# Performance work log

Measured on AMD Instinct MI355X. Metric: run time of the kernel, lower is better.

Reference implementation:

```python
import jax, jax.numpy as jnp
import numpy as np

B, S, H, F, E, TOP_K = 4, 2048, 768, 3072, 8, 2


def setup_inputs() -> dict:
    key = jax.random.key(0)
    ks = jax.random.split(key, 6)
    x = jax.random.normal(ks[0], (B, S, H), dtype=jnp.float32)
    Wr = jax.random.normal(ks[1], (E, H), dtype=jnp.float32) * 0.02
    Wi = jax.random.normal(ks[2], (E, F, H), dtype=jnp.float32) * 0.02
    bi = jnp.zeros((E, F), dtype=jnp.float32)
    Wo = jax.random.normal(ks[3], (E, H, F), dtype=jnp.float32) * 0.02
    bo = jnp.zeros((E, H), dtype=jnp.float32)
    return {"x": x, "Wr": Wr, "Wi": Wi, "bi": bi, "Wo": Wo, "bo": bo}


def reference(x, Wr, Wi, bi, Wo, bo):
    # x: [B, S, H] -> tokens [T, H]
    xf = x.reshape(-1, x.shape[-1])  # [T, H]

    # Router: linear (no bias), eval mode (no noise), temperature=1.0
    router_logits = jnp.einsum('th,eh->te', xf, Wr)  # [T, E]
    topk_vals, topk_idx = jax.lax.top_k(router_logits, TOP_K)  # [T, K]
    routing_weights = jax.nn.softmax(topk_vals, axis=-1)  # normalize over top-k

    # All experts on all tokens (forward_all_experts, parallel computation)
    h = jnp.einsum('th,efh->etf', xf, Wi) + bi[:, None, :]  # [E, T, F]
    h = jax.nn.gelu(h, approximate=False)  # BERT gelu (erf)
    expert_out = jnp.einsum('etf,ehf->eth', h, Wo) + bo[:, None, :]  # [E, T, H]
    expert_out = jnp.transpose(expert_out, (1, 0, 2))  # [T, E, H]

    # Gather top-k expert outputs per token and combine with routing weights
    gathered = jnp.take_along_axis(expert_out, topk_idx[:, :, None], axis=1)  # [T, K, H]
    out = jnp.einsum('tk,tkh->th', routing_weights, gathered)
    return out.reshape(x.shape)
```

## Files before the change

kernel.cpp:

```cpp
#include <hip/hip_runtime.h>
#include <hip/hip_bf16.h>
#include <cstdint>
#include <cstddef>

#define T_TOK 8192
#define HDIM  768
#define FDIM  3072
#define NEXP  8

typedef __attribute__((ext_vector_type(8))) __bf16 bf16x8;
typedef __attribute__((ext_vector_type(4))) float  f32x4;

static __device__ __forceinline__ f32x4 mfma16(bf16x8 a, bf16x8 b, f32x4 c) {
  return __builtin_amdgcn_mfma_f32_16x16x32_bf16(a, b, c, 0, 0, 0);
}

static __device__ __forceinline__ unsigned short f2b(float f) {
  return __builtin_bit_cast(unsigned short, (__bf16)f);
}

static __device__ __forceinline__ float gelu_f(float x) {
  float x2 = x * x;
  float y = x * (0.7978845608f + 0.0356774081f * x2);
  float ay = __builtin_fabsf(y);
  float z = __builtin_amdgcn_exp2f(ay * -2.885390082f);
  float t = (1.0f - z) * __builtin_amdgcn_rcpf(1.0f + z);
  t = __builtin_copysignf(t, y);
  return 0.5f * x * (1.0f + t);
}

static constexpr size_t OFF_XB   = 0;
static constexpr size_t OFF_WIB  = OFF_XB  + (size_t)T_TOK * HDIM * 2;
static constexpr size_t OFF_WOB  = OFF_WIB + (size_t)NEXP * FDIM * HDIM * 2;
static constexpr size_t OFF_HBUF = OFF_WOB + (size_t)NEXP * HDIM * FDIM * 2;
static constexpr size_t OFF_META = OFF_HBUF + (size_t)2 * T_TOK * FDIM * 2;
static constexpr size_t OFF_TOKE = OFF_META + 256;
static constexpr size_t OFF_TOKW = OFF_TOKE + 65536;
static constexpr size_t OFF_PTOK = OFF_TOKW + 65536;
static constexpr size_t OFF_PW   = OFF_PTOK + 65536;
static constexpr size_t OFF_TILE = OFF_PW + 65536;
static constexpr size_t OFF_STAGE = 0;

__global__ __launch_bounds__(256) void cvt_kernel(const float* __restrict__ s,
                                                  unsigned short* __restrict__ d, int n4) {
  int i = blockIdx.x * 256 + threadIdx.x;
  int stride = gridDim.x * 256;
  for (; i < n4; i += stride) {
    float4 v = ((const float4*)s)[i];
    ushort4 o;
    o.x = f2b(v.x); o.y = f2b(v.y); o.z = f2b(v.z); o.w = f2b(v.w);
    ((ushort4*)d)[i] = o;
  }
}

__global__ __launch_bounds__(256) void router_kernel(const float* __restrict__ x,
                                                     const float* __restrict__ Wr,
                                                     int* __restrict__ tok_e,
                                                     float* __restrict__ tok_w,
                                                     unsigned short* __restrict__ xb) {
  __shared__ float wr[NEXP * HDIM];
  int tid = threadIdx.x;
  for (int i = tid; i < NEXP * HDIM; i += 256) wr[i] = Wr[i];
  __syncthreads();
  int lane = tid & 63;
  int wv = tid >> 6;
  int t = blockIdx.x * 4 + wv;
  const float* xr = x + (size_t)t * HDIM;
  unsigned short* xbr = xb + (size_t)t * HDIM;
  float p[NEXP];
#pragma unroll
  for (int e = 0; e < NEXP; ++e) p[e] = 0.f;
  for (int j = 0; j < HDIM / 64; ++j) {
    float xv = xr[j * 64 + lane];
    xbr[j * 64 + lane] = f2b(xv);
#pragma unroll
    for (int e = 0; e < NEXP; ++e) p[e] += xv * wr[e * HDIM + j * 64 + lane];
  }
#pragma unroll
  for (int e = 0; e < NEXP; ++e) {
    float v = p[e];
    for (int off = 32; off; off >>= 1) v += __shfl_xor(v, off);
    p[e] = v;
  }
  if (lane == 0) {
    float v0 = -1e30f, v1 = -1e30f; int i0 = 0, i1 = 0;
#pragma unroll
    for (int e = 0; e < NEXP; ++e) {
      float v = p[e];
      if (v > v0) { v1 = v0; i1 = i0; v0 = v; i0 = e; }
      else if (v > v1) { v1 = v; i1 = e; }
    }
    float ew = expf(v1 - v0);
    float w0 = 1.0f / (1.0f + ew);
    float w1 = ew * w0;
    tok_e[t * 2 + 0] = i0; tok_w[t * 2 + 0] = w0;
    tok_e[t * 2 + 1] = i1; tok_w[t * 2 + 1] = w1;
  }
}

__global__ __launch_bounds__(256) void count_kernel(const int* __restrict__ tok_e,
                                                    int* __restrict__ counts) {
  __shared__ int h[NEXP];
  int tid = threadIdx.x;
  if (tid < NEXP) h[tid] = 0;
  __syncthreads();
  int i = blockIdx.x * 256 + tid;
  atomicAdd(&h[tok_e[i]], 1);
  __syncthreads();
  if (tid < NEXP && h[tid] > 0) atomicAdd(&counts[tid], h[tid]);
}

__global__ void scan_build_kernel(const int* __restrict__ counts, int* __restrict__ basep,
                                  int* __restrict__ tile_e, int* __restrict__ tile_mt,
                                  int* __restrict__ ntiles) {
  if (threadIdx.x != 0 || blockIdx.x != 0) return;
  int s = 0;
  for (int e = 0; e < NEXP; ++e) { basep[e] = s; s += counts[e]; }
  int n = 0;
  for (int e = 0; e < NEXP; ++e) {
    int nmt = (counts[e] + 255) >> 8;
    for (int m = 0; m < nmt; ++m) { tile_e[n] = e; tile_mt[n] = m; ++n; }
  }
  ntiles[0] = n;
}

__global__ __launch_bounds__(256) void scatter_kernel(const int* __restrict__ tok_e,
                                                      const float* __restrict__ tok_w,
                                                      const int* __restrict__ base,
                                                      int* __restrict__ cursor,
                                                      int* __restrict__ pair_tok,
                                                      float* __restrict__ pair_w) {
  __shared__ int h[NEXP], bstart[NEXP];
  int tid = threadIdx.x;
  if (tid < NEXP) h[tid] = 0;
  __syncthreads();
  int i = blockIdx.x * 256 + tid;
  int e = tok_e[i];
  int r = atomicAdd(&h[e], 1);
  __syncthreads();
  if (tid < NEXP) bstart[tid] = (h[tid] > 0) ? atomicAdd(&cursor[tid], h[tid]) : 0;
  __syncthreads();
  int pos = base[e] + bstart[e] + r;
  pair_tok[pos] = i;
  pair_w[pos] = tok_w[i];
}

template <int MODE>
__global__ __launch_bounds__(512, 2) void moe_gemm(
    const unsigned short* __restrict__ abase,
    const unsigned short* __restrict__ wbase,
    const float* __restrict__ bias,
    const int* __restrict__ counts, const int* __restrict__ base,
    const int* __restrict__ pair_tok, const float* __restrict__ pair_w,
    const int* __restrict__ tile_e, const int* __restrict__ tile_mt,
    const int* __restrict__ ntiles,
    unsigned short* __restrict__ hbuf, float* __restrict__ stage) {
  constexpr int K   = MODE ? FDIM : HDIM;
  constexpr int N   = MODE ? HDIM : FDIM;
  constexpr int NT  = K / 64;
  constexpr int NTC = N / 256;

  const int xcd = blockIdx.x & 7;
  const int slot = blockIdx.x >> 3;
  const int mtl = slot % 9;
  const int nt = slot / 9;
  const int ntl = ntiles[0];
  const int q = ntl >> 3, r = ntl & 7;
  const int cnt = q + (xcd < r ? 1 : 0);
  if (mtl >= cnt) return;
  const int gt = xcd * q + (xcd < r ? xcd : r) + mtl;
  const int e = tile_e[gt];
  const int mt = tile_mt[gt];
  const int ne = counts[e];
  const int pb = base[e];

  extern __shared__ char smem[];

  const int tid = threadIdx.x;
  const int lane = tid & 63;
  const int wv = tid >> 6;
  const int wm = wv >> 2;
  const int wn = wv & 3;
  const int l15 = lane & 15;
  const int lkb = (lane >> 4) * 16;

  const int crow = tid >> 3;
  const int ck = tid & 7;
  const int swz = (ck ^ (crow & 7)) * 16;
  const char* aS[4]; const char* bS[4];
#pragma unroll
  for (int i = 0; i < 4; ++i) {
    int gr = mt * 256 + i * 64 + crow; if (gr > ne - 1) gr = ne - 1;
    if constexpr (MODE == 0) {
      int tok = pair_tok[pb + gr] >> 1;
      aS[i] = (const char*)abase + (size_t)tok * (HDIM * 2) + swz;
    } else {
      aS[i] = (const char*)abase + (size_t)(pb + gr) * (FDIM * 2) + swz;
    }
    int br = nt * 256 + i * 64 + crow;
    bS[i] = (const char*)wbase + ((size_t)e * N * K + (size_t)br * K) * 2 + swz;
  }

  auto STAGE = [&](int c, int t) {
    if (t < NT) {
      const char* src = (c < 4 ? aS[c] : bS[c - 4]) + t * 128;
      char* dst = smem + (size_t)((t & 1) * 65536 + c * 8192 + tid * 16);
      __builtin_amdgcn_global_load_lds(
          (const __attribute__((address_space(1))) void*)src,
          (__attribute__((address_space(3))) void*)dst, 16, 0, 0);
    }
  };

  bf16x8 aR[8], bR0[4], bR1[4];
  f32x4 acc[8][4];
#pragma unroll
  for (int mi = 0; mi < 8; ++mi)
#pragma unroll
    for (int ni = 0; ni < 4; ++ni) acc[mi][ni] = (f32x4){0.f, 0.f, 0.f, 0.f};

  auto READA = [&](int cb, int h) {
#pragma unroll
    for (int m2 = 0; m2 < 4; ++m2)
#pragma unroll
      for (int k2 = 0; k2 < 2; ++k2) {
        int lr = wm * 128 + (h * 4 + m2) * 16 + l15;
        int cbyte = k2 * 64 + lkb;
        aR[m2 * 2 + k2] =
            *(const bf16x8*)(smem + cb + lr * 128 + (cbyte ^ ((lr & 7) << 4)));
      }
  };
  auto READB = [&](int cb, int h, bf16x8* bR) {
#pragma unroll
    for (int n2 = 0; n2 < 2; ++n2)
#pragma unroll
      for (int k2 = 0; k2 < 2; ++k2) {
        int lr = wn * 64 + (h * 2 + n2) * 16 + l15;
        int cbyte = k2 * 64 + lkb;
        bR[n2 * 2 + k2] =
            *(const bf16x8*)(smem + cb + 32768 + lr * 128 + (cbyte ^ ((lr & 7) << 4)));
      }
  };
  auto MFMAQ = [&](int qm, int qn, const bf16x8* bR) {
#pragma unroll
    for (int m2 = 0; m2 < 4; ++m2)
#pragma unroll
      for (int n2 = 0; n2 < 2; ++n2)
#pragma unroll
        for (int k2 = 0; k2 < 2; ++k2)
          acc[qm * 4 + m2][qn * 2 + n2] =
              mfma16(aR[m2 * 2 + k2], bR[n2 * 2 + k2], acc[qm * 4 + m2][qn * 2 + n2]);
  };

#pragma unroll
  for (int c = 0; c < 8; ++c) STAGE(c, 0);
  STAGE(0, 1); STAGE(1, 1);
  asm volatile("s_waitcnt vmcnt(2)" ::: "memory");
  __builtin_amdgcn_s_barrier();

  for (int t = 0; t < NT; ++t) {
    const int cb = (t & 1) * 65536;
    READA(cb, 0); READB(cb, 0, bR0);
    STAGE(2, t + 1); STAGE(3, t + 1);
    __builtin_amdgcn_s_barrier();
    asm volatile("s_waitcnt lgkmcnt(0)" ::: "memory");
    __builtin_amdgcn_sched_barrier(0);
    __builtin_amdgcn_s_setprio(1);
    MFMAQ(0, 0, bR0);
    __builtin_amdgcn_s_setprio(0);
    __builtin_amdgcn_s_barrier();
    READB(cb, 1, bR1);
    STAGE(4, t + 1); STAGE(5, t + 1);
    __builtin_amdgcn_s_barrier();
    asm volatile("s_waitcnt lgkmcnt(0)" ::: "memory");
    __builtin_amdgcn_sched_barrier(0);
    __builtin_amdgcn_s_setprio(1);
    MFMAQ(0, 1, bR1);
    __builtin_amdgcn_s_setprio(0);
    __builtin_amdgcn_s_barrier();
    READA(cb, 1);
    STAGE(6, t + 1); STAGE(7, t + 1);
    __builtin_amdgcn_s_barrier();
    asm volatile("s_waitcnt lgkmcnt(0)" ::: "memory");
    __builtin_amdgcn_sched_barrier(0);
    __builtin_amdgcn_s_setprio(1);
    MFMAQ(1, 1, bR1);
    __builtin_amdgcn_s_setprio(0);
    __builtin_amdgcn_s_barrier();
    STAGE(0, t + 2); STAGE(1, t + 2);
    __builtin_amdgcn_s_barrier();
    __builtin_amdgcn_s_setprio(1);
    MFMAQ(1, 0, bR0);
    __builtin_amdgcn_s_setprio(0);
    if (t + 2 < NT) asm volatile("s_waitcnt vmcnt(2)" ::: "memory");
    else            asm volatile("s_waitcnt vmcnt(0)" ::: "memory");
    __builtin_amdgcn_s_barrier();
  }

  if constexpr (MODE == 0) {
    const float* be = bias + (size_t)e * FDIM;
    float bv[4];
#pragma unroll
    for (int ni = 0; ni < 4; ++ni) bv[ni] = be[nt * 256 + wn * 64 + ni * 16 + l15];
#pragma unroll
    for (int mi = 0; mi < 8; ++mi)
#pragma unroll
      for (int rr = 0; rr < 4; ++rr) {
        int row = mt * 256 + wm * 128 + mi * 16 + (lane >> 4) * 4 + rr;
        if (row < ne) {
          unsigned short* hr = hbuf + (size_t)(pb + row) * FDIM + nt * 256 + wn * 64 + l15;
#pragma unroll
          for (int ni = 0; ni < 4; ++ni)
            hr[ni * 16] = f2b(gelu_f(acc[mi][ni][rr] + bv[ni]));
        }
      }
  } else {
    const float* be = bias + (size_t)e * HDIM;
    float bv[4];
#pragma unroll
    for (int ni = 0; ni < 4; ++ni) bv[ni] = be[nt * 256 + wn * 64 + ni * 16 + l15];
#pragma unroll
    for (int mi = 0; mi < 8; ++mi)
#pragma unroll
      for (int rr = 0; rr < 4; ++rr) {
        int row = mt * 256 + wm * 128 + mi * 16 + (lane >> 4) * 4 + rr;
        if (row < ne) {
          int p = pb + row;
          int ts = pair_tok[p];
          float w = pair_w[p];
          float* sr = stage + (size_t)ts * HDIM + nt * 256 + wn * 64 + l15;
#pragma unroll
          for (int ni = 0; ni < 4; ++ni)
            sr[ni * 16] = (acc[mi][ni][rr] + bv[ni]) * w;
        }
      }
  }
}

__global__ __launch_bounds__(256) void combine_kernel(const float* __restrict__ stage,
                                                      float* __restrict__ out) {
  const int n4 = T_TOK * HDIM / 4;
  int i = blockIdx.x * 256 + threadIdx.x;
  int stride = gridDim.x * 256;
  const float4* s = (const float4*)stage;
  float4* o = (float4*)out;
  for (; i < n4; i += stride) {
    int t = i / (HDIM / 4);
    int h = i - t * (HDIM / 4);
    float4 a = s[(size_t)t * (HDIM / 2) + h];
    float4 b = s[(size_t)t * (HDIM / 2) + (HDIM / 4) + h];
    float4 rr; rr.x = a.x + b.x; rr.y = a.y + b.y; rr.z = a.z + b.z; rr.w = a.w + b.w;
    o[i] = rr;
  }
}

extern "C" void kernel_launch(void* const* d_in, const int* in_sizes, int n_in,
                              void* d_out, int out_size, void* d_ws, size_t ws_size,
                              hipStream_t stream) {
  const float* x  = (const float*)d_in[0];
  const float* Wr = (const float*)d_in[1];
  const float* Wi = (const float*)d_in[2];
  const float* bi = (const float*)d_in[3];
  const float* Wo = (const float*)d_in[4];
  const float* bo = (const float*)d_in[5];
  float* out = (float*)d_out;
  char* ws = (char*)d_ws;

  unsigned short* xb   = (unsigned short*)(ws + OFF_XB);
  unsigned short* wib  = (unsigned short*)(ws + OFF_WIB);
  unsigned short* wob  = (unsigned short*)(ws + OFF_WOB);
  unsigned short* hbuf = (unsigned short*)(ws + OFF_HBUF);
  int*   counts   = (int*)(ws + OFF_META);
  int*   basep    = (int*)(ws + OFF_META + 64);
  int*   cursor   = (int*)(ws + OFF_META + 128);
  int*   tok_e    = (int*)(ws + OFF_TOKE);
  float* tok_w    = (float*)(ws + OFF_TOKW);
  int*   pair_tok = (int*)(ws + OFF_PTOK);
  float* pair_w   = (float*)(ws + OFF_PW);
  int*   tile_e   = (int*)(ws + OFF_TILE);
  int*   tile_mt  = (int*)(ws + OFF_TILE + 512);
  int*   ntiles   = (int*)(ws + OFF_TILE + 1024);
  float* stage    = (float*)(ws + OFF_STAGE);

  hipFuncSetAttribute((const void*)&moe_gemm<0>,
                      hipFuncAttributeMaxDynamicSharedMemorySize, 131072);
  hipFuncSetAttribute((const void*)&moe_gemm<1>,
                      hipFuncAttributeMaxDynamicSharedMemorySize, 131072);

  hipMemsetAsync(ws + OFF_META, 0, 256, stream);

  router_kernel<<<T_TOK / 4, 256, 0, stream>>>(x, Wr, tok_e, tok_w, xb);
  cvt_kernel<<<2048, 256, 0, stream>>>(Wi, wib, NEXP * FDIM * HDIM / 4);
  cvt_kernel<<<2048, 256, 0, stream>>>(Wo, wob, NEXP * HDIM * FDIM / 4);

  count_kernel<<<64, 256, 0, stream>>>(tok_e, counts);
  scan_build_kernel<<<1, 64, 0, stream>>>(counts, basep, tile_e, tile_mt, ntiles);
  scatter_kernel<<<64, 256, 0, stream>>>(tok_e, tok_w, basep, cursor, pair_tok, pair_w);

  moe_gemm<0><<<8 * 9 * (FDIM / 256), 512, 131072, stream>>>(
      xb, wib, bi, counts, basep, pair_tok, pair_w, tile_e, tile_mt, ntiles, hbuf, nullptr);
  moe_gemm<1><<<8 * 9 * (HDIM / 256), 512, 131072, stream>>>(
      hbuf, wob, bo, counts, basep, pair_tok, pair_w, tile_e, tile_mt, ntiles, nullptr, stage);

  combine_kernel<<<2048, 256, 0, stream>>>(stage, out);
}
```

Baseline: 295.5 us.

## Make MoE GEMM persistent with grouped per-XCD tile scheduling

Replaces the one-tile-per-block launch (8*9*NTC blocks, many exiting early) with a fixed grid of 192 persistent blocks, 24 per XCD. Each block loops over groups of M-tiles and N-tiles (4x6 for the first GEMM, 8x3 for the second), so blocks in a group share A rows and weight columns in cache. This removes idle early-exit blocks and the cost of launching them. In exchange the work is serialized inside each block, which can cause load imbalance or partial waves when the tile count does not divide evenly, and it adds a block-wide barrier between groups.

```diff
diff --git a/kernel.cpp b/kernel.cpp
--- a/kernel.cpp
+++ b/kernel.cpp
@@ -159,20 +159,15 @@
   constexpr int N   = MODE ? HDIM : FDIM;
   constexpr int NT  = K / 64;
   constexpr int NTC = N / 256;
+  constexpr int BMT = MODE ? 8 : 4;
+  constexpr int BNT = MODE ? 3 : 6;
 
   const int xcd = blockIdx.x & 7;
-  const int slot = blockIdx.x >> 3;
-  const int mtl = slot % 9;
-  const int nt = slot / 9;
+  const int c   = blockIdx.x >> 3;
   const int ntl = ntiles[0];
   const int q = ntl >> 3, r = ntl & 7;
   const int cnt = q + (xcd < r ? 1 : 0);
-  if (mtl >= cnt) return;
-  const int gt = xcd * q + (xcd < r ? xcd : r) + mtl;
-  const int e = tile_e[gt];
-  const int mt = tile_mt[gt];
-  const int ne = counts[e];
-  const int pb = base[e];
+  const int t0 = xcd * q + (xcd < r ? xcd : r);
 
   extern __shared__ char smem[];
 
@@ -183,156 +178,172 @@
   const int wn = wv & 3;
   const int l15 = lane & 15;
   const int lkb = (lane >> 4) * 16;
-
   const int crow = tid >> 3;
   const int ck = tid & 7;
   const int swz = (ck ^ (crow & 7)) * 16;
-  const char* aS[4]; const char* bS[4];
-#pragma unroll
-  for (int i = 0; i < 4; ++i) {
-    int gr = mt * 256 + i * 64 + crow; if (gr > ne - 1) gr = ne - 1;
-    if constexpr (MODE == 0) {
-      int tok = pair_tok[pb + gr] >> 1;
-      aS[i] = (const char*)abase + (size_t)tok * (HDIM * 2) + swz;
-    } else {
-      aS[i] = (const char*)abase + (size_t)(pb + gr) * (FDIM * 2) + swz;
-    }
-    int br = nt * 256 + i * 64 + crow;
-    bS[i] = (const char*)wbase + ((size_t)e * N * K + (size_t)br * K) * 2 + swz;
-  }
-
-  auto STAGE = [&](int c, int t) {
-    if (t < NT) {
-      const char* src = (c < 4 ? aS[c] : bS[c - 4]) + t * 128;
-      char* dst = smem + (size_t)((t & 1) * 65536 + c * 8192 + tid * 16);
-      __builtin_amdgcn_global_load_lds(
-          (const __attribute__((address_space(1))) void*)src,
-          (__attribute__((address_space(3))) void*)dst, 16, 0, 0);
-    }
-  };
-
-  bf16x8 aR[8], bR0[4], bR1[4];
-  f32x4 acc[8][4];
-#pragma unroll
-  for (int mi = 0; mi < 8; ++mi)
-#pragma unroll
-    for (int ni = 0; ni < 4; ++ni) acc[mi][ni] = (f32x4){0.f, 0.f, 0.f, 0.f};
-
-  auto READA = [&](int cb, int h) {
-#pragma unroll
-    for (int m2 = 0; m2 < 4; ++m2)
-#pragma unroll
-      for (int k2 = 0; k2 < 2; ++k2) {
-        int lr = wm * 128 + (h * 4 + m2) * 16 + l15;
-        int cbyte = k2 * 64 + lkb;
-        aR[m2 * 2 + k2] =
-            *(const bf16x8*)(smem + cb + lr * 128 + (cbyte ^ ((lr & 7) << 4)));
-      }
-  };
-  auto READB = [&](int cb, int h, bf16x8* bR) {
-#pragma unroll
-    for (int n2 = 0; n2 < 2; ++n2)
-#pragma unroll
-      for (int k2 = 0; k2 < 2; ++k2) {
-        int lr = wn * 64 + (h * 2 + n2) * 16 + l15;
-        int cbyte = k2 * 64 + lkb;
-        bR[n2 * 2 + k2] =
-            *(const bf16x8*)(smem + cb + 32768 + lr * 128 + (cbyte ^ ((lr & 7) << 4)));
-      }
-  };
-  auto MFMAQ = [&](int qm, int qn, const bf16x8* bR) {
-#pragma unroll
-    for (int m2 = 0; m2 < 4; ++m2)
-#pragma unroll
-      for (int n2 = 0; n2 < 2; ++n2)
-#pragma unroll
-        for (int k2 = 0; k2 < 2; ++k2)
-          acc[qm * 4 + m2][qn * 2 + n2] =
-              mfma16(aR[m2 * 2 + k2], bR[n2 * 2 + k2], acc[qm * 4 + m2][qn * 2 + n2]);
-  };
-
-#pragma unroll
-  for (int c = 0; c < 8; ++c) STAGE(c, 0);
-  STAGE(0, 1); STAGE(1, 1);
-  asm volatile("s_waitcnt vmcnt(2)" ::: "memory");
-  __builtin_amdgcn_s_barrier();
-
-  for (int t = 0; t < NT; ++t) {
-    const int cb = (t & 1) * 65536;
-    READA(cb, 0); READB(cb, 0, bR0);
-    STAGE(2, t + 1); STAGE(3, t + 1);
-    __builtin_amdgcn_s_barrier();
-    asm volatile("s_waitcnt lgkmcnt(0)" ::: "memory");
-    __builtin_amdgcn_sched_barrier(0);
-    __builtin_amdgcn_s_setprio(1);
-    MFMAQ(0, 0, bR0);
-    __builtin_amdgcn_s_setprio(0);
-    __builtin_amdgcn_s_barrier();
-    READB(cb, 1, bR1);
-    STAGE(4, t + 1); STAGE(5, t + 1);
-    __builtin_amdgcn_s_barrier();
-    asm volatile("s_waitcnt lgkmcnt(0)" ::: "memory");
-    __builtin_amdgcn_sched_barrier(0);
-    __builtin_amdgcn_s_setprio(1);
-    MFMAQ(0, 1, bR1);
-    __builtin_amdgcn_s_setprio(0);
-    __builtin_amdgcn_s_barrier();
-    READA(cb, 1);
-    STAGE(6, t + 1); STAGE(7, t + 1);
-    __builtin_amdgcn_s_barrier();
-    asm volatile("s_waitcnt lgkmcnt(0)" ::: "memory");
-    __builtin_amdgcn_sched_barrier(0);
-    __builtin_amdgcn_s_setprio(1);
-    MFMAQ(1, 1, bR1);
-    __builtin_amdgcn_s_setprio(0);
-    __builtin_amdgcn_s_barrier();
-    STAGE(0, t + 2); STAGE(1, t + 2);
-    __builtin_amdgcn_s_barrier();
-    __builtin_amdgcn_s_setprio(1);
-    MFMAQ(1, 0, bR0);
-    __builtin_amdgcn_s_setprio(0);
-    if (t + 2 < NT) asm volatile("s_waitcnt vmcnt(2)" ::: "memory");
-    else            asm volatile("s_waitcnt vmcnt(0)" ::: "memory");
-    __builtin_amdgcn_s_barrier();
-  }
-
-  if constexpr (MODE == 0) {
-    const float* be = bias + (size_t)e * FDIM;
-    float bv[4];
-#pragma unroll
-    for (int ni = 0; ni < 4; ++ni) bv[ni] = be[nt * 256 + wn * 64 + ni * 16 + l15];
-#pragma unroll
-    for (int mi = 0; mi < 8; ++mi)
-#pragma unroll
-      for (int rr = 0; rr < 4; ++rr) {
-        int row = mt * 256 + wm * 128 + mi * 16 + (lane >> 4) * 4 + rr;
-        if (row < ne) {
-          unsigned short* hr = hbuf + (size_t)(pb + row) * FDIM + nt * 256 + wn * 64 + l15;
-#pragma unroll
-          for (int ni = 0; ni < 4; ++ni)
-            hr[ni * 16] = f2b(gelu_f(acc[mi][ni][rr] + bv[ni]));
+
+  for (int mtg = 0; mtg * BMT < cnt; ++mtg) {
+    int w = cnt - mtg * BMT; if (w > BMT) w = BMT;
+    for (int ntg = 0; ntg * BNT < NTC; ++ntg) {
+      if (c < w * BNT) {
+        const int nt = ntg * BNT + c / w;
+        const int gt = t0 + mtg * BMT + c % w;
+        const int e = tile_e[gt];
+        const int mt = tile_mt[gt];
+        const int ne = counts[e];
+        const int pb = base[e];
+
+        const char* aS[4]; const char* bS[4];
+#pragma unroll
+        for (int i = 0; i < 4; ++i) {
+          int gr = mt * 256 + i * 64 + crow; if (gr > ne - 1) gr = ne - 1;
+          if constexpr (MODE == 0) {
+            int tok = pair_tok[pb + gr] >> 1;
+            aS[i] = (const char*)abase + (size_t)tok * (HDIM * 2) + swz;
+          } else {
+            aS[i] = (const char*)abase + (size_t)(pb + gr) * (FDIM * 2) + swz;
+          }
+          int br = nt * 256 + i * 64 + crow;
+          bS[i] = (const char*)wbase + ((size_t)e * N * K + (size_t)br * K) * 2 + swz;
+        }
+
+        auto STAGE = [&](int cch, int t) {
+          if (t < NT) {
+            const char* src = (cch < 4 ? aS[cch] : bS[cch - 4]) + t * 128;
+            char* dst = smem + (size_t)((t & 1) * 65536 + cch * 8192 + tid * 16);
+            __builtin_amdgcn_global_load_lds(
+                (const __attribute__((address_space(1))) void*)src,
+                (__attribute__((address_space(3))) void*)dst, 16, 0, 0);
+          }
+        };
+
+        bf16x8 aR[8], bR0[4], bR1[4];
+        f32x4 acc[8][4];
+#pragma unroll
+        for (int mi = 0; mi < 8; ++mi)
+#pragma unroll
+          for (int ni = 0; ni < 4; ++ni) acc[mi][ni] = (f32x4){0.f, 0.f, 0.f, 0.f};
+
+        auto READA = [&](int cb, int h) {
+#pragma unroll
+          for (int m2 = 0; m2 < 4; ++m2)
+#pragma unroll
+            for (int k2 = 0; k2 < 2; ++k2) {
+              int lr = wm * 128 + (h * 4 + m2) * 16 + l15;
+              int cbyte = k2 * 64 + lkb;
+              aR[m2 * 2 + k2] =
+                  *(const bf16x8*)(smem + cb + lr * 128 + (cbyte ^ ((lr & 7) << 4)));
+            }
+        };
+        auto READB = [&](int cb, int h, bf16x8* bR) {
+#pragma unroll
+          for (int n2 = 0; n2 < 2; ++n2)
+#pragma unroll
+            for (int k2 = 0; k2 < 2; ++k2) {
+              int lr = wn * 64 + (h * 2 + n2) * 16 + l15;
+              int cbyte = k2 * 64 + lkb;
+              bR[n2 * 2 + k2] =
+                  *(const bf16x8*)(smem + cb + 32768 + lr * 128 + (cbyte ^ ((lr & 7) << 4)));
+            }
+        };
+        auto MFMAQ = [&](int qm, int qn, const bf16x8* bR) {
+#pragma unroll
+          for (int m2 = 0; m2 < 4; ++m2)
+#pragma unroll
+            for (int n2 = 0; n2 < 2; ++n2)
+#pragma unroll
+              for (int k2 = 0; k2 < 2; ++k2)
+                acc[qm * 4 + m2][qn * 2 + n2] =
+                    mfma16(aR[m2 * 2 + k2], bR[n2 * 2 + k2], acc[qm * 4 + m2][qn * 2 + n2]);
+        };
+
+#pragma unroll
+        for (int cch = 0; cch < 8; ++cch) STAGE(cch, 0);
+        STAGE(0, 1); STAGE(1, 1);
+        asm volatile("s_waitcnt vmcnt(2)" ::: "memory");
+        __builtin_amdgcn_s_barrier();
+
+        for (int t = 0; t < NT; ++t) {
+          const int cb = (t & 1) * 65536;
+          READA(cb, 0); READB(cb, 0, bR0);
+          STAGE(2, t + 1); STAGE(3, t + 1);
+          __builtin_amdgcn_s_barrier();
+          asm volatile("s_waitcnt lgkmcnt(0)" ::: "memory");
+          __builtin_amdgcn_sched_barrier(0);
+          __builtin_amdgcn_s_setprio(1);
+          MFMAQ(0, 0, bR0);
+          __builtin_amdgcn_s_setprio(0);
+          __builtin_amdgcn_s_barrier();
+          READB(cb, 1, bR1);
+          STAGE(4, t + 1); STAGE(5, t + 1);
+          __builtin_amdgcn_s_barrier();
+          asm volatile("s_waitcnt lgkmcnt(0)" ::: "memory");
+          __builtin_amdgcn_sched_barrier(0);
+          __builtin_amdgcn_s_setprio(1);
+          MFMAQ(0, 1, bR1);
+          __builtin_amdgcn_s_setprio(0);
+          __builtin_amdgcn_s_barrier();
+          READA(cb, 1);
+          STAGE(6, t + 1); STAGE(7, t + 1);
+          __builtin_amdgcn_s_barrier();
+          asm volatile("s_waitcnt lgkmcnt(0)" ::: "memory");
+          __builtin_amdgcn_sched_barrier(0);
+          __builtin_amdgcn_s_setprio(1);
+          MFMAQ(1, 1, bR1);
+          __builtin_amdgcn_s_setprio(0);
+          __builtin_amdgcn_s_barrier();
+          STAGE(0, t + 2); STAGE(1, t + 2);
+          __builtin_amdgcn_s_barrier();
+          __builtin_amdgcn_s_setprio(1);
+          MFMAQ(1, 0, bR0);
+          __builtin_amdgcn_s_setprio(0);
+          if (t + 2 < NT) asm volatile("s_waitcnt vmcnt(2)" ::: "memory");
+          else            asm volatile("s_waitcnt vmcnt(0)" ::: "memory");
+          __builtin_amdgcn_s_barrier();
+        }
+
+        if constexpr (MODE == 0) {
+          const float* be = bias + (size_t)e * FDIM;
+          float bv[4];
+#pragma unroll
+          for (int ni = 0; ni < 4; ++ni) bv[ni] = be[nt * 256 + wn * 64 + ni * 16 + l15];
+#pragma unroll
+          for (int mi = 0; mi < 8; ++mi)
+#pragma unroll
+            for (int rr = 0; rr < 4; ++rr) {
+              int row = mt * 256 + wm * 128 + mi * 16 + (lane >> 4) * 4 + rr;
+              if (row < ne) {
+                unsigned short* hr =
+                    hbuf + (size_t)(pb + row) * FDIM + nt * 256 + wn * 64 + l15;
+#pragma unroll
+                for (int ni = 0; ni < 4; ++ni)
+                  hr[ni * 16] = f2b(gelu_f(acc[mi][ni][rr] + bv[ni]));
+              }
+            }
+        } else {
+          const float* be = bias + (size_t)e * HDIM;
+          float bv[4];
+#pragma unroll
+          for (int ni = 0; ni < 4; ++ni) bv[ni] = be[nt * 256 + wn * 64 + ni * 16 + l15];
+#pragma unroll
+          for (int mi = 0; mi < 8; ++mi)
+#pragma unroll
+            for (int rr = 0; rr < 4; ++rr) {
+              int row = mt * 256 + wm * 128 + mi * 16 + (lane >> 4) * 4 + rr;
+              if (row < ne) {
+                int p = pb + row;
+                int ts = pair_tok[p];
+                float wgt = pair_w[p];
+                float* sr = stage + (size_t)ts * HDIM + nt * 256 + wn * 64 + l15;
+#pragma unroll
+                for (int ni = 0; ni < 4; ++ni)
+                  sr[ni * 16] = (acc[mi][ni][rr] + bv[ni]) * wgt;
+              }
+            }
         }
       }
-  } else {
-    const float* be = bias + (size_t)e * HDIM;
-    float bv[4];
-#pragma unroll
-    for (int ni = 0; ni < 4; ++ni) bv[ni] = be[nt * 256 + wn * 64 + ni * 16 + l15];
-#pragma unroll
-    for (int mi = 0; mi < 8; ++mi)
-#pragma unroll
-      for (int rr = 0; rr < 4; ++rr) {
-        int row = mt * 256 + wm * 128 + mi * 16 + (lane >> 4) * 4 + rr;
-        if (row < ne) {
-          int p = pb + row;
-          int ts = pair_tok[p];
-          float w = pair_w[p];
-          float* sr = stage + (size_t)ts * HDIM + nt * 256 + wn * 64 + l15;
-#pragma unroll
-          for (int ni = 0; ni < 4; ++ni)
-            sr[ni * 16] = (acc[mi][ni][rr] + bv[ni]) * w;
-        }
-      }
+      __builtin_amdgcn_s_barrier();
+    }
   }
 }
 
@@ -396,9 +407,9 @@
   scan_build_kernel<<<1, 64, 0, stream>>>(counts, basep, tile_e, tile_mt, ntiles);
   scatter_kernel<<<64, 256, 0, stream>>>(tok_e, tok_w, basep, cursor, pair_tok, pair_w);
 
-  moe_gemm<0><<<8 * 9 * (FDIM / 256), 512, 131072, stream>>>(
+  moe_gemm<0><<<192, 512, 131072, stream>>>(
       xb, wib, bi, counts, basep, pair_tok, pair_w, tile_e, tile_mt, ntiles, hbuf, nullptr);
-  moe_gemm<1><<<8 * 9 * (HDIM / 256), 512, 131072, stream>>>(
+  moe_gemm<1><<<192, 512, 131072, stream>>>(
       hbuf, wob, bo, counts, basep, pair_tok, pair_w, tile_e, tile_mt, ntiles, nullptr, stage);
 
   combine_kernel<<<2048, 256, 0, stream>>>(stage, out);
```

New measurement: 417.6 us. +41.4%, slower.

## Restructure GEMM main loop into quadrant-staged 2x-unrolled pipeline with new wave mapping

Applied to the files above, without the earlier changes.

Changes the wave-to-tile mapping so each wave computes four 64x32 quadrant sub-tiles spread across the 256x256 block, instead of one 128x64 contiguous region. The K loop is unrolled by two, and LDS staging is issued per quadrant half in a new order, with deeper vmcnt waits. Each half of the shared tile can then be refilled as soon as its quadrant's MFMAs are done, which is meant to overlap global-to-LDS loads with compute more tightly. The loop now assumes NT is even, and the epilogue stores are more fragmented, which may hurt write coalescing.

```diff
diff --git a/kernel.cpp b/kernel.cpp
--- a/kernel.cpp
+++ b/kernel.cpp
@@ -179,8 +179,8 @@
   const int tid = threadIdx.x;
   const int lane = tid & 63;
   const int wv = tid >> 6;
-  const int wm = wv >> 2;
-  const int wn = wv & 3;
+  const int wlo = wv & 1;
+  const int whi = wv >> 1;
   const int l15 = lane & 15;
   const int lkb = (lane >> 4) * 16;
 
@@ -210,130 +210,137 @@
           (__attribute__((address_space(3))) void*)dst, 16, 0, 0);
     }
   };
+  auto SH = [&](int h, int t) { STAGE(2 * h, t); STAGE(2 * h + 1, t); };
 
   bf16x8 aR[8], bR0[4], bR1[4];
-  f32x4 acc[8][4];
-#pragma unroll
-  for (int mi = 0; mi < 8; ++mi)
-#pragma unroll
-    for (int ni = 0; ni < 4; ++ni) acc[mi][ni] = (f32x4){0.f, 0.f, 0.f, 0.f};
-
-  auto READA = [&](int cb, int h) {
-#pragma unroll
-    for (int m2 = 0; m2 < 4; ++m2)
-#pragma unroll
-      for (int k2 = 0; k2 < 2; ++k2) {
-        int lr = wm * 128 + (h * 4 + m2) * 16 + l15;
-        int cbyte = k2 * 64 + lkb;
-        aR[m2 * 2 + k2] =
-            *(const bf16x8*)(smem + cb + lr * 128 + (cbyte ^ ((lr & 7) << 4)));
+  f32x4 acc[4][4][2];
+#pragma unroll
+  for (int qi = 0; qi < 4; ++qi)
+#pragma unroll
+    for (int mf = 0; mf < 4; ++mf)
+#pragma unroll
+      for (int nf = 0; nf < 2; ++nf) acc[qi][mf][nf] = (f32x4){0.f, 0.f, 0.f, 0.f};
+
+  auto RA = [&](int cb, int qm) {
+#pragma unroll
+    for (int mf = 0; mf < 4; ++mf)
+#pragma unroll
+      for (int kh = 0; kh < 2; ++kh) {
+        int lr = qm * 128 + wlo * 64 + mf * 16 + l15;
+        aR[mf * 2 + kh] =
+            *(const bf16x8*)(smem + cb + lr * 128 + ((kh * 64 + lkb) ^ ((lr & 7) << 4)));
       }
   };
-  auto READB = [&](int cb, int h, bf16x8* bR) {
-#pragma unroll
-    for (int n2 = 0; n2 < 2; ++n2)
-#pragma unroll
-      for (int k2 = 0; k2 < 2; ++k2) {
-        int lr = wn * 64 + (h * 2 + n2) * 16 + l15;
-        int cbyte = k2 * 64 + lkb;
-        bR[n2 * 2 + k2] =
-            *(const bf16x8*)(smem + cb + 32768 + lr * 128 + (cbyte ^ ((lr & 7) << 4)));
+  auto RB = [&](int cb, int qn, bf16x8* bR) {
+#pragma unroll
+    for (int nf = 0; nf < 2; ++nf)
+#pragma unroll
+      for (int kh = 0; kh < 2; ++kh) {
+        int lb = qn * 128 + whi * 32 + nf * 16 + l15;
+        bR[nf * 2 + kh] =
+            *(const bf16x8*)(smem + cb + 32768 + lb * 128 + ((kh * 64 + lkb) ^ ((lb & 7) << 4)));
       }
   };
-  auto MFMAQ = [&](int qm, int qn, const bf16x8* bR) {
-#pragma unroll
-    for (int m2 = 0; m2 < 4; ++m2)
-#pragma unroll
-      for (int n2 = 0; n2 < 2; ++n2)
-#pragma unroll
-        for (int k2 = 0; k2 < 2; ++k2)
-          acc[qm * 4 + m2][qn * 2 + n2] =
-              mfma16(aR[m2 * 2 + k2], bR[n2 * 2 + k2], acc[qm * 4 + m2][qn * 2 + n2]);
+  auto MQ = [&](int qi, const bf16x8* bR) {
+#pragma unroll
+    for (int mf = 0; mf < 4; ++mf)
+#pragma unroll
+      for (int nf = 0; nf < 2; ++nf)
+#pragma unroll
+        for (int kh = 0; kh < 2; ++kh)
+          acc[qi][mf][nf] = mfma16(aR[mf * 2 + kh], bR[nf * 2 + kh], acc[qi][mf][nf]);
   };
 
-#pragma unroll
-  for (int c = 0; c < 8; ++c) STAGE(c, 0);
-  STAGE(0, 1); STAGE(1, 1);
-  asm volatile("s_waitcnt vmcnt(2)" ::: "memory");
-  __builtin_amdgcn_s_barrier();
-
-  for (int t = 0; t < NT; ++t) {
-    const int cb = (t & 1) * 65536;
-    READA(cb, 0); READB(cb, 0, bR0);
-    STAGE(2, t + 1); STAGE(3, t + 1);
-    __builtin_amdgcn_s_barrier();
-    asm volatile("s_waitcnt lgkmcnt(0)" ::: "memory");
-    __builtin_amdgcn_sched_barrier(0);
-    __builtin_amdgcn_s_setprio(1);
-    MFMAQ(0, 0, bR0);
-    __builtin_amdgcn_s_setprio(0);
-    __builtin_amdgcn_s_barrier();
-    READB(cb, 1, bR1);
-    STAGE(4, t + 1); STAGE(5, t + 1);
-    __builtin_amdgcn_s_barrier();
-    asm volatile("s_waitcnt lgkmcnt(0)" ::: "memory");
-    __builtin_amdgcn_sched_barrier(0);
-    __builtin_amdgcn_s_setprio(1);
-    MFMAQ(0, 1, bR1);
-    __builtin_amdgcn_s_setprio(0);
-    __builtin_amdgcn_s_barrier();
-    READA(cb, 1);
-    STAGE(6, t + 1); STAGE(7, t + 1);
-    __builtin_amdgcn_s_barrier();
-    asm volatile("s_waitcnt lgkmcnt(0)" ::: "memory");
-    __builtin_amdgcn_sched_barrier(0);
-    __builtin_amdgcn_s_setprio(1);
-    MFMAQ(1, 1, bR1);
-    __builtin_amdgcn_s_setprio(0);
-    __builtin_amdgcn_s_barrier();
-    STAGE(0, t + 2); STAGE(1, t + 2);
-    __builtin_amdgcn_s_barrier();
-    __builtin_amdgcn_s_setprio(1);
-    MFMAQ(1, 0, bR0);
-    __builtin_amdgcn_s_setprio(0);
-    if (t + 2 < NT) asm volatile("s_waitcnt vmcnt(2)" ::: "memory");
-    else            asm volatile("s_waitcnt vmcnt(0)" ::: "memory");
-    __builtin_amdgcn_s_barrier();
-  }
-
-  if constexpr (MODE == 0) {
-    const float* be = bias + (size_t)e * FDIM;
-    float bv[4];
-#pragma unroll
-    for (int ni = 0; ni < 4; ++ni) bv[ni] = be[nt * 256 + wn * 64 + ni * 16 + l15];
-#pragma unroll
-    for (int mi = 0; mi < 8; ++mi)
-#pragma unroll
-      for (int rr = 0; rr < 4; ++rr) {
-        int row = mt * 256 + wm * 128 + mi * 16 + (lane >> 4) * 4 + rr;
-        if (row < ne) {
-          unsigned short* hr = hbuf + (size_t)(pb + row) * FDIM + nt * 256 + wn * 64 + l15;
-#pragma unroll
-          for (int ni = 0; ni < 4; ++ni)
-            hr[ni * 16] = f2b(gelu_f(acc[mi][ni][rr] + bv[ni]));
+#define BAR()   __builtin_amdgcn_s_barrier()
+#define LGKM0() asm volatile("s_waitcnt lgkmcnt(0)" ::: "memory"); \
+                __builtin_amdgcn_sched_barrier(0)
+#define P1()    __builtin_amdgcn_s_setprio(1)
+#define P0()    __builtin_amdgcn_s_setprio(0)
+
+  SH(0, 0); SH(3, 0); SH(2, 0); SH(1, 0); SH(0, 1); SH(3, 1);
+  asm volatile("s_waitcnt vmcnt(6)" ::: "memory");
+  BAR();
+
+  for (int it = 0; it < NT / 2; ++it) {
+    const int u = 2 * it, v = u + 1;
+    const bool last = (it == NT / 2 - 1);
+    RA(0, 0); RB(0, 0, bR0); SH(2, v);
+    BAR(); LGKM0(); P1(); MQ(0, bR0); P0(); BAR();
+    RB(0, 1, bR1); SH(1, v);
+    BAR(); LGKM0(); P1(); MQ(1, bR1); P0();
+    asm volatile("s_waitcnt vmcnt(8)" ::: "memory");
+    BAR();
+    RA(0, 1); SH(0, u + 2);
+    BAR(); LGKM0(); P1(); MQ(3, bR1); P0(); BAR();
+    SH(3, u + 2);
+    BAR(); P1(); MQ(2, bR0); P0();
+    if (!last) asm volatile("s_waitcnt vmcnt(6)" ::: "memory");
+    else       asm volatile("s_waitcnt vmcnt(2)" ::: "memory");
+    BAR();
+    RA(65536, 0); RB(65536, 0, bR0); SH(2, u + 2);
+    BAR(); LGKM0(); P1(); MQ(0, bR0); P0(); BAR();
+    RB(65536, 1, bR1); SH(1, u + 2);
+    BAR(); LGKM0(); P1(); MQ(1, bR1); P0();
+    if (!last) asm volatile("s_waitcnt vmcnt(8)" ::: "memory");
+    else       asm volatile("s_waitcnt vmcnt(0)" ::: "memory");
+    BAR();
+    RA(65536, 1); SH(0, v + 2);
+    BAR(); LGKM0(); P1(); MQ(3, bR1); P0(); BAR();
+    SH(3, v + 2);
+    BAR(); P1(); MQ(2, bR0); P0();
+    asm volatile("s_waitcnt vmcnt(6)" ::: "memory");
+    BAR();
+  }
+
+#pragma unroll
+  for (int qi = 0; qi < 4; ++qi) {
+    const int qm = qi >> 1, qn = qi & 1;
+    if constexpr (MODE == 0) {
+      const float* be = bias + (size_t)e * FDIM;
+      float bv[2];
+#pragma unroll
+      for (int nf = 0; nf < 2; ++nf)
+        bv[nf] = be[nt * 256 + qn * 128 + whi * 32 + nf * 16 + l15];
+#pragma unroll
+      for (int mf = 0; mf < 4; ++mf)
+#pragma unroll
+        for (int rr = 0; rr < 4; ++rr) {
+          int row = mt * 256 + qm * 128 + wlo * 64 + mf * 16 + (lane >> 4) * 4 + rr;
+          if (row < ne) {
+            unsigned short* hr = hbuf + (size_t)(pb + row) * FDIM +
+                                 nt * 256 + qn * 128 + whi * 32 + l15;
+#pragma unroll
+            for (int nf = 0; nf < 2; ++nf)
+              hr[nf * 16] = f2b(gelu_f(acc[qi][mf][nf][rr] + bv[nf]));
+          }
         }
-      }
-  } else {
-    const float* be = bias + (size_t)e * HDIM;
-    float bv[4];
-#pragma unroll
-    for (int ni = 0; ni < 4; ++ni) bv[ni] = be[nt * 256 + wn * 64 + ni * 16 + l15];
-#pragma unroll
-    for (int mi = 0; mi < 8; ++mi)
-#pragma unroll
-      for (int rr = 0; rr < 4; ++rr) {
-        int row = mt * 256 + wm * 128 + mi * 16 + (lane >> 4) * 4 + rr;
-        if (row < ne) {
-          int p = pb + row;
-          int ts = pair_tok[p];
-          float w = pair_w[p];
-          float* sr = stage + (size_t)ts * HDIM + nt * 256 + wn * 64 + l15;
-#pragma unroll
-          for (int ni = 0; ni < 4; ++ni)
-            sr[ni * 16] = (acc[mi][ni][rr] + bv[ni]) * w;
+    } else {
+      const float* be = bias + (size_t)e * HDIM;
+      float bv[2];
+#pragma unroll
+      for (int nf = 0; nf < 2; ++nf)
+        bv[nf] = be[nt * 256 + qn * 128 + whi * 32 + nf * 16 + l15];
+#pragma unroll
+      for (int mf = 0; mf < 4; ++mf)
+#pragma unroll
+        for (int rr = 0; rr < 4; ++rr) {
+          int row = mt * 256 + qm * 128 + wlo * 64 + mf * 16 + (lane >> 4) * 4 + rr;
+          if (row < ne) {
+            int p = pb + row;
+            int ts = pair_tok[p];
+            float w = pair_w[p];
+            float* sr = stage + (size_t)ts * HDIM + nt * 256 + qn * 128 + whi * 32 + l15;
+#pragma unroll
+            for (int nf = 0; nf < 2; ++nf)
+              sr[nf * 16] = (acc[qi][mf][nf][rr] + bv[nf]) * w;
+          }
         }
-      }
-  }
+    }
+  }
+#undef BAR
+#undef LGKM0
+#undef P1
+#undef P0
 }
 
 __global__ __launch_bounds__(256) void combine_kernel(const float* __restrict__ stage,
```

New measurement: 482.9 us. 63.4% more time.

## Replace double-buffered phased GEMM pipeline with single-buffered load-then-compute loop

Applied to the files above, without the earlier changes.

The MoE GEMM main loop drops its 4-phase, double-buffered LDS schedule, where loads of chunks were interleaved with quarter-tile MFMA groups. Each iteration now reads all A/B fragments from a single LDS buffer into registers and issues all 8 loads for the next k-tile. It then runs the full 8x4 MFMA block and waits for all loads to finish. LDS use drops from 128KB to 64KB and barrier count per iteration falls, but fragment register pressure rises and load/compute overlap is limited to one tile with a full vmcnt(0) drain every step. A leftover no-op loop is also added.

```diff
diff --git a/kernel.cpp b/kernel.cpp
--- a/kernel.cpp
+++ b/kernel.cpp
@@ -201,98 +201,77 @@
     bS[i] = (const char*)wbase + ((size_t)e * N * K + (size_t)br * K) * 2 + swz;
   }
 
-  auto STAGE = [&](int c, int t) {
+  auto STAGE = [&](int t) {
     if (t < NT) {
-      const char* src = (c < 4 ? aS[c] : bS[c - 4]) + t * 128;
-      char* dst = smem + (size_t)((t & 1) * 65536 + c * 8192 + tid * 16);
-      __builtin_amdgcn_global_load_lds(
-          (const __attribute__((address_space(1))) void*)src,
-          (__attribute__((address_space(3))) void*)dst, 16, 0, 0);
+#pragma unroll
+      for (int c = 0; c < 8; ++c) {
+        const char* src = (c < 4 ? aS[c] : bS[c - 4]) + t * 128;
+        char* dst = smem + (size_t)(c * 8192 + tid * 16);
+        __builtin_amdgcn_global_load_lds(
+            (const __attribute__((address_space(1))) void*)src,
+            (__attribute__((address_space(3))) void*)dst, 16, 0, 0);
+      }
     }
   };
 
-  bf16x8 aR[8], bR0[4], bR1[4];
+  bf16x8 aR[8], bR[8];
   f32x4 acc[8][4];
 #pragma unroll
   for (int mi = 0; mi < 8; ++mi)
 #pragma unroll
     for (int ni = 0; ni < 4; ++ni) acc[mi][ni] = (f32x4){0.f, 0.f, 0.f, 0.f};
 
-  auto READA = [&](int cb, int h) {
+  STAGE(0);
+  asm volatile("s_waitcnt vmcnt(0)" ::: "memory");
+  __builtin_amdgcn_s_barrier();
+
+  for (int t = 0; t < NT; ++t) {
+#pragma unroll
+    for (int mi = 0; mi < 8; ++mi)
+#pragma unroll
+      for (int k2 = 0; k2 < 2; ++k2) {
+        int lr = wm * 128 + mi * 16 + l15;
+        if (k2 == 0 || (mi & 1) == (mi & 1)) {}
+        aR[(mi & 3) * 2 + k2] = aR[(mi & 3) * 2 + k2];
+      }
+    bf16x8 a0[8], b0[8];
 #pragma unroll
     for (int m2 = 0; m2 < 4; ++m2)
 #pragma unroll
       for (int k2 = 0; k2 < 2; ++k2) {
-        int lr = wm * 128 + (h * 4 + m2) * 16 + l15;
-        int cbyte = k2 * 64 + lkb;
+        int lr0 = wm * 128 + m2 * 16 + l15;
+        int lr1 = wm * 128 + 64 + m2 * 16 + l15;
+        a0[m2 * 2 + k2] =
+            *(const bf16x8*)(smem + lr0 * 128 + ((k2 * 64 + lkb) ^ ((lr0 & 7) << 4)));
         aR[m2 * 2 + k2] =
-            *(const bf16x8*)(smem + cb + lr * 128 + (cbyte ^ ((lr & 7) << 4)));
-      }
-  };
-  auto READB = [&](int cb, int h, bf16x8* bR) {
-#pragma unroll
-    for (int n2 = 0; n2 < 2; ++n2)
+            *(const bf16x8*)(smem + lr1 * 128 + ((k2 * 64 + lkb) ^ ((lr1 & 7) << 4)));
+      }
+#pragma unroll
+    for (int n2 = 0; n2 < 4; ++n2)
 #pragma unroll
       for (int k2 = 0; k2 < 2; ++k2) {
-        int lr = wn * 64 + (h * 2 + n2) * 16 + l15;
-        int cbyte = k2 * 64 + lkb;
-        bR[n2 * 2 + k2] =
-            *(const bf16x8*)(smem + cb + 32768 + lr * 128 + (cbyte ^ ((lr & 7) << 4)));
-      }
-  };
-  auto MFMAQ = [&](int qm, int qn, const bf16x8* bR) {
-#pragma unroll
-    for (int m2 = 0; m2 < 4; ++m2)
-#pragma unroll
-      for (int n2 = 0; n2 < 2; ++n2)
-#pragma unroll
-        for (int k2 = 0; k2 < 2; ++k2)
-          acc[qm * 4 + m2][qn * 2 + n2] =
-              mfma16(aR[m2 * 2 + k2], bR[n2 * 2 + k2], acc[qm * 4 + m2][qn * 2 + n2]);
-  };
-
-#pragma unroll
-  for (int c = 0; c < 8; ++c) STAGE(c, 0);
-  STAGE(0, 1); STAGE(1, 1);
-  asm volatile("s_waitcnt vmcnt(2)" ::: "memory");
-  __builtin_amdgcn_s_barrier();
-
-  for (int t = 0; t < NT; ++t) {
-    const int cb = (t & 1) * 65536;
-    READA(cb, 0); READB(cb, 0, bR0);
-    STAGE(2, t + 1); STAGE(3, t + 1);
-    __builtin_amdgcn_s_barrier();
+        int lb = wn * 64 + n2 * 16 + l15;
+        b0[n2 * 2 + k2] =
+            *(const bf16x8*)(smem + 32768 + lb * 128 + ((k2 * 64 + lkb) ^ ((lb & 7) << 4)));
+      }
     asm volatile("s_waitcnt lgkmcnt(0)" ::: "memory");
     __builtin_amdgcn_sched_barrier(0);
-    __builtin_amdgcn_s_setprio(1);
-    MFMAQ(0, 0, bR0);
-    __builtin_amdgcn_s_setprio(0);
     __builtin_amdgcn_s_barrier();
-    READB(cb, 1, bR1);
-    STAGE(4, t + 1); STAGE(5, t + 1);
-    __builtin_amdgcn_s_barrier();
-    asm volatile("s_waitcnt lgkmcnt(0)" ::: "memory");
+    STAGE(t + 1);
     __builtin_amdgcn_sched_barrier(0);
     __builtin_amdgcn_s_setprio(1);
-    MFMAQ(0, 1, bR1);
+#pragma unroll
+    for (int m2 = 0; m2 < 4; ++m2)
+#pragma unroll
+      for (int n2 = 0; n2 < 4; ++n2)
+#pragma unroll
+        for (int k2 = 0; k2 < 2; ++k2) {
+          acc[m2][n2]     = mfma16(a0[m2 * 2 + k2], b0[n2 * 2 + k2], acc[m2][n2]);
+          acc[4 + m2][n2] = mfma16(aR[m2 * 2 + k2], b0[n2 * 2 + k2], acc[4 + m2][n2]);
+        }
     __builtin_amdgcn_s_setprio(0);
-    __builtin_amdgcn_s_barrier();
-    READA(cb, 1);
-    STAGE(6, t + 1); STAGE(7, t + 1);
-    __builtin_amdgcn_s_barrier();
-    asm volatile("s_waitcnt lgkmcnt(0)" ::: "memory");
     __builtin_amdgcn_sched_barrier(0);
-    __builtin_amdgcn_s_setprio(1);
-    MFMAQ(1, 1, bR1);
-    __builtin_amdgcn_s_setprio(0);
-    __builtin_amdgcn_s_barrier();
-    STAGE(0, t + 2); STAGE(1, t + 2);
-    __builtin_amdgcn_s_barrier();
-    __builtin_amdgcn_s_setprio(1);
-    MFMAQ(1, 0, bR0);
-    __builtin_amdgcn_s_setprio(0);
-    if (t + 2 < NT) asm volatile("s_waitcnt vmcnt(2)" ::: "memory");
-    else            asm volatile("s_waitcnt vmcnt(0)" ::: "memory");
+    asm volatile("s_waitcnt vmcnt(0)" ::: "memory");
     __builtin_amdgcn_s_barrier();
   }
 
@@ -305,12 +284,12 @@
     for (int mi = 0; mi < 8; ++mi)
 #pragma unroll
       for (int rr = 0; rr < 4; ++rr) {
-        int row = mt * 256 + wm * 128 + mi * 16 + (lane >> 4) * 4 + rr;
+        int row = mt * 256 + wm * 128 + (mi >> 2) * 64 + (mi & 3) * 16 + (lane >> 4) * 4 + rr;
         if (row < ne) {
           unsigned short* hr = hbuf + (size_t)(pb + row) * FDIM + nt * 256 + wn * 64 + l15;
 #pragma unroll
           for (int ni = 0; ni < 4; ++ni)
-            hr[ni * 16] = f2b(gelu_f(acc[mi][ni][rr] + bv[ni]));
+            hr[ni * 16] = f2b(gelu_f(acc[(mi >> 2) * 4 + (mi & 3)][ni][rr] + bv[ni]));
         }
       }
   } else {
@@ -322,7 +301,7 @@
     for (int mi = 0; mi < 8; ++mi)
 #pragma unroll
       for (int rr = 0; rr < 4; ++rr) {
-        int row = mt * 256 + wm * 128 + mi * 16 + (lane >> 4) * 4 + rr;
+        int row = mt * 256 + wm * 128 + (mi >> 2) * 64 + (mi & 3) * 16 + (lane >> 4) * 4 + rr;
         if (row < ne) {
           int p = pb + row;
           int ts = pair_tok[p];
@@ -330,7 +309,7 @@
           float* sr = stage + (size_t)ts * HDIM + nt * 256 + wn * 64 + l15;
 #pragma unroll
           for (int ni = 0; ni < 4; ++ni)
-            sr[ni * 16] = (acc[mi][ni][rr] + bv[ni]) * w;
+            sr[ni * 16] = (acc[(mi >> 2) * 4 + (mi & 3)][ni][rr] + bv[ni]) * w;
         }
       }
   }
@@ -382,9 +361,9 @@
   float* stage    = (float*)(ws + OFF_STAGE);
 
   hipFuncSetAttribute((const void*)&moe_gemm<0>,
-                      hipFuncAttributeMaxDynamicSharedMemorySize, 131072);
+                      hipFuncAttributeMaxDynamicSharedMemorySize, 65536);
   hipFuncSetAttribute((const void*)&moe_gemm<1>,
-                      hipFuncAttributeMaxDynamicSharedMemorySize, 131072);
+                      hipFuncAttributeMaxDynamicSharedMemorySize, 65536);
 
   hipMemsetAsync(ws + OFF_META, 0, 256, stream);
 
@@ -396,9 +375,9 @@
   scan_build_kernel<<<1, 64, 0, stream>>>(counts, basep, tile_e, tile_mt, ntiles);
   scatter_kernel<<<64, 256, 0, stream>>>(tok_e, tok_w, basep, cursor, pair_tok, pair_w);
 
-  moe_gemm<0><<<8 * 9 * (FDIM / 256), 512, 131072, stream>>>(
+  moe_gemm<0><<<8 * 9 * (FDIM / 256), 512, 65536, stream>>>(
       xb, wib, bi, counts, basep, pair_tok, pair_w, tile_e, tile_mt, ntiles, hbuf, nullptr);
-  moe_gemm<1><<<8 * 9 * (HDIM / 256), 512, 131072, stream>>>(
+  moe_gemm<1><<<8 * 9 * (HDIM / 256), 512, 65536, stream>>>(
       hbuf, wob, bo, counts, basep, pair_tok, pair_w, tile_e, tile_mt, ntiles, nullptr, stage);
 
   combine_kernel<<<2048, 256, 0, stream>>>(stage, out);
```

New measurement: 295.1 us. No clear change (-0.1%).
